# Performance work log

Measured on AMD Instinct MI355X. Metric: run time of the kernel, lower is better.

The kernel has to match this reference:

```python
import jax, jax.numpy as jnp
import numpy as np

DIM_MODEL = 1024
NUM_HEADS = 16
DIM_HEAD = 64
B, S = 2, 2048


def setup_inputs() -> dict:
    key = jax.random.key(0)
    ks = jax.random.split(key, 10)
    scale = 1.0 / np.sqrt(DIM_MODEL)
    inp = {
        "x": jax.random.normal(ks[0], (B, S, DIM_MODEL), dtype=jnp.float32),
        "padding_mask": jax.random.randint(ks[1], (B, S), 0, 2, dtype=jnp.int32),
        "Wq": jax.random.normal(ks[2], (DIM_MODEL, DIM_MODEL), dtype=jnp.float32) * scale,
        "bq": jnp.zeros((DIM_MODEL,), dtype=jnp.float32),
        "Wk": jax.random.normal(ks[3], (DIM_MODEL, DIM_MODEL), dtype=jnp.float32) * scale,
        "bk": jnp.zeros((DIM_MODEL,), dtype=jnp.float32),
        "Wv": jax.random.normal(ks[4], (DIM_MODEL, DIM_MODEL), dtype=jnp.float32) * scale,
        "bv": jnp.zeros((DIM_MODEL,), dtype=jnp.float32),
        "Wo": jax.random.normal(ks[5], (DIM_MODEL, DIM_MODEL), dtype=jnp.float32) * scale,
        "bo": jnp.zeros((DIM_MODEL,), dtype=jnp.float32),
    }
    return inp


def reference(x, padding_mask, Wq, bq, Wk, bk, Wv, bv, Wo, bo):
    b, s, _ = x.shape
    dot_scale = jnp.sqrt(jnp.asarray(DIM_HEAD, dtype=x.dtype))
    # projections -> (b, h, s, d)
    q = (x @ Wq + bq).reshape(b, s, NUM_HEADS, DIM_HEAD).transpose(0, 2, 1, 3)
    k = (x @ Wk + bk).reshape(b, s, NUM_HEADS, DIM_HEAD).transpose(0, 2, 1, 3)
    v = (x @ Wv + bv).reshape(b, s, NUM_HEADS, DIM_HEAD).transpose(0, 2, 1, 3)
    # scores (b, h, s, s)
    scores = jnp.einsum("bhqd,bhkd->bhqk", q, k) / dot_scale
    mask = (padding_mask == 1)[:, None, None, :]  # (b,1,1,s) over key positions
    scores = jnp.where(mask, -jnp.inf, scores)
    attn = jax.nn.softmax(scores, axis=-1)
    out = jnp.einsum("bhqk,bhkd->bhqd", attn, v)
    out = out.transpose(0, 2, 1, 3).reshape(b, s, NUM_HEADS * DIM_HEAD)
    return out @ Wo + bo
```

## Files before the change

kernel.cpp:

```cpp
#include <hip/hip_runtime.h>
#include <hip/hip_bf16.h>
#include <stdint.h>
#include <math.h>

#define D_MODEL 1024
#define NHEAD   16
#define DHEAD   64
#define BATCH   2
#define SEQ     2048
#define M_TOK   (BATCH * SEQ)

#define QSCALE 0.18033688011112042f

typedef __attribute__((ext_vector_type(8))) short   short8;
typedef __attribute__((ext_vector_type(8))) __bf16  bf16x8;
typedef __attribute__((ext_vector_type(4))) float   f32x4;

__device__ inline short f2bf(float f) {
  unsigned int u = __builtin_bit_cast(unsigned int, f);
  unsigned int r = (u + 0x7FFFu + ((u >> 16) & 1u)) >> 16;
  return (short)(unsigned short)r;
}
__device__ inline short f2bf_fast(float f) {
  unsigned int u = __builtin_bit_cast(unsigned int, f);
  return (short)(unsigned short)((u + 0x8000u) >> 16);
}

__device__ inline void gl_lds16(const void* g, void* l) {
  __builtin_amdgcn_global_load_lds((__attribute__((address_space(1))) void*)(g),
                                   (__attribute__((address_space(3))) void*)(l),
                                   16, 0, 0);
}

__device__ inline bf16x8 lds_frag(const short* p) {
  return *(const bf16x8*)(p);
}
__device__ inline bf16x8 lds_frag64(const short* p) {
  union { bf16x8 v; short4 h[2]; } u;
  u.h[0] = *(const short4*)(p);
  u.h[1] = *(const short4*)(p + 4);
  return u.v;
}

__global__ __launch_bounds__(256) void prep(const float* __restrict__ x,
                                            short* __restrict__ xb,
                                            const float* __restrict__ w0,
                                            const float* __restrict__ w1,
                                            const float* __restrict__ w2,
                                            const float* __restrict__ w3,
                                            short* __restrict__ out) {
  const int t = threadIdx.x;
  if (blockIdx.z == 4) {
    size_t base = ((size_t)blockIdx.y * 16 + blockIdx.x) * 16384;
    const float* in = x + base;
    short* o = xb + base;
#pragma unroll
    for (int i = 0; i < 16; ++i) {
      f32x4 v = *(const f32x4*)(in + (size_t)t * 4 + i * 1024);
      short4 s4;
      s4.x = f2bf(v[0]); s4.y = f2bf(v[1]); s4.z = f2bf(v[2]); s4.w = f2bf(v[3]);
      *(short4*)(o + (size_t)t * 4 + i * 1024) = s4;
    }
    return;
  }
  __shared__ short tile[64][72];
  const float* W = blockIdx.z == 0 ? w0 : blockIdx.z == 1 ? w1 : blockIdx.z == 2 ? w2 : w3;
  short* O = out + (size_t)blockIdx.z * (D_MODEL * (size_t)D_MODEL);
  int n0 = blockIdx.x * 64, k0 = blockIdx.y * 64;
#pragma unroll
  for (int i = 0; i < 16; ++i) {
    int idx = t + 256 * i;
    int r = idx >> 6, c = idx & 63;
    tile[r][c] = f2bf(W[(size_t)(k0 + r) * D_MODEL + n0 + c]);
  }
  __syncthreads();
#pragma unroll
  for (int i = 0; i < 16; ++i) {
    int idx = t + 256 * i;
    int r = idx >> 6, c = idx & 63;
    O[(size_t)(n0 + r) * D_MODEL + k0 + c] = tile[c][r];
  }
}

template <bool OUTF32, bool VT, int TN>
__global__ __launch_bounds__(256) void gemm128(const short* __restrict__ A,
                                               const short* __restrict__ Bt_base,
                                               const float* __restrict__ b0,
                                               const float* __restrict__ b1,
                                               const float* __restrict__ b2,
                                               void* __restrict__ out_base,
                                               short* __restrict__ vt,
                                               const int* __restrict__ pm) {
  constexpr int NI = TN / 32;
  const int z = blockIdx.z;
  const short* Bt   = Bt_base + (size_t)z * (D_MODEL * (size_t)D_MODEL);
  const float* bias = (z == 0) ? b0 : (z == 1) ? b1 : b2;

  __shared__ short As[128 * 64];
  __shared__ short Bs[TN * 64];

  const int t = threadIdx.x;
  const int lane = t & 63;
  const int wid = t >> 6;
  const int wm = (wid >> 1) * 64, wn = (wid & 1) * (TN / 2);
  const int m0 = blockIdx.x * 128, n0 = blockIdx.y * TN;
  const int cl = lane & 15, q = lane >> 4;
  const int sw = cl & 7;

  f32x4 acc[4][NI];
#pragma unroll
  for (int i = 0; i < 4; ++i)
#pragma unroll
    for (int j = 0; j < NI; ++j) acc[i][j] = 0.0f;

  for (int k0 = 0; k0 < D_MODEL; k0 += 64) {
    __syncthreads();
#pragma unroll
    for (int i = 0; i < 4; ++i) {
      int c = t + 256 * i;
      int row = c >> 3, cp = c & 7;
      int col = ((cp ^ (row & 7)) * 8);
      gl_lds16(A + (size_t)(m0 + row) * D_MODEL + k0 + col, (void*)(As + c * 8));
    }
#pragma unroll
    for (int i = 0; i < NI; ++i) {
      int c = t + 256 * i;
      int row = c >> 3, cp = c & 7;
      int col = ((cp ^ (row & 7)) * 8);
      gl_lds16(Bt + (size_t)(n0 + row) * D_MODEL + k0 + col, (void*)(Bs + c * 8));
    }
    __syncthreads();

    bf16x8 af[4][2], bfr[NI][2];
#pragma unroll
    for (int mi = 0; mi < 4; ++mi) {
      af[mi][0] = lds_frag(As + (wm + mi * 16 + cl) * 64 + (q ^ sw) * 8);
      af[mi][1] = lds_frag(As + (wm + mi * 16 + cl) * 64 + ((4 + q) ^ sw) * 8);
    }
#pragma unroll
    for (int ni = 0; ni < NI; ++ni) {
      bfr[ni][0] = lds_frag(Bs + (wn + ni * 16 + cl) * 64 + (q ^ sw) * 8);
      bfr[ni][1] = lds_frag(Bs + (wn + ni * 16 + cl) * 64 + ((4 + q) ^ sw) * 8);
    }
#pragma unroll
    for (int mi = 0; mi < 4; ++mi)
#pragma unroll
      for (int ni = 0; ni < NI; ++ni) {
        acc[mi][ni] = __builtin_amdgcn_mfma_f32_16x16x32_bf16(af[mi][0], bfr[ni][0], acc[mi][ni], 0, 0, 0);
        acc[mi][ni] = __builtin_amdgcn_mfma_f32_16x16x32_bf16(af[mi][1], bfr[ni][1], acc[mi][ni], 0, 0, 0);
      }
  }

  const float oscale = (VT && z == 0) ? QSCALE : 1.0f;
  int4 mm[4];
  if (VT && z == 2) {
#pragma unroll
    for (int mi = 0; mi < 4; ++mi) {
      int rbase = m0 + wm + mi * 16 + q * 4;
      mm[mi] = *(const int4*)(pm + (size_t)(rbase >> 11) * SEQ + (rbase & (SEQ - 1)));
    }
  }
#pragma unroll
  for (int ni = 0; ni < NI; ++ni) {
    int col = n0 + wn + ni * 16 + cl;
    float bv = bias[col];
#pragma unroll
    for (int mi = 0; mi < 4; ++mi) {
      int rbase = m0 + wm + mi * 16 + q * 4;
      if (VT && z == 2) {
        short4 o4;
        o4.x = (mm[mi].x == 1) ? (short)0 : f2bf_fast(acc[mi][ni][0] + bv);
        o4.y = (mm[mi].y == 1) ? (short)0 : f2bf_fast(acc[mi][ni][1] + bv);
        o4.z = (mm[mi].z == 1) ? (short)0 : f2bf_fast(acc[mi][ni][2] + bv);
        o4.w = (mm[mi].w == 1) ? (short)0 : f2bf_fast(acc[mi][ni][3] + bv);
        int btok = rbase >> 11;
        int s    = rbase & (SEQ - 1);
        *(short4*)(vt + (size_t)btok * ((size_t)D_MODEL * SEQ) + (size_t)col * SEQ + s) = o4;
      } else {
#pragma unroll
        for (int r = 0; r < 4; ++r) {
          float v = (acc[mi][ni][r] + bv) * oscale;
          size_t idx = (size_t)(rbase + r) * D_MODEL + col;
          if (OUTF32) {
            ((float*)out_base)[idx] = v;
          } else {
            short* out = (short*)out_base + (size_t)z * ((size_t)M_TOK * D_MODEL);
            out[idx] = f2bf_fast(v);
          }
        }
      }
    }
  }
}

__global__ __launch_bounds__(512) void attn_flash(const short* __restrict__ Q,
                                                  const short* __restrict__ K,
                                                  const short* __restrict__ Vt,
                                                  const int*   __restrict__ mask,
                                                  short* __restrict__ ctx) {
  const int qb = blockIdx.x;
  const int h  = blockIdx.y;
  const int b  = blockIdx.z;

  __shared__ __align__(16) short QPs[17408];
  __shared__ __align__(16) short Ks[2 * 64 * 64];
  __shared__ __align__(16) short Vts[2 * 64 * 64];
  __shared__ __align__(16) short Usall[SEQ];

  const int t = threadIdx.x;
  const int lane = t & 63;
  const int wid = t >> 6;
  const int wg  = wid >> 1;
  const int kvh = wid & 1;
  const int cl = lane & 15, q = lane >> 4;
  const int sw = cl & 7;

  const size_t rowQ0 = (size_t)b * SEQ + (size_t)qb * 128;
  const size_t rowK0 = (size_t)b * SEQ;
  const size_t vbase = ((size_t)b * D_MODEL + h * DHEAD) * SEQ;

  const int srow = t >> 3, scp = t & 7;
  const int scol = (scp ^ (srow & 7)) * 8;
  const short* Kg0 = K + (rowK0 + srow) * D_MODEL + h * DHEAD + scol;
  const short* Kg1 = K + (rowK0 + 1024 + srow) * D_MODEL + h * DHEAD + scol;
  const short* Vg0 = Vt + vbase + (size_t)srow * SEQ + scol;
  const short* Vg1 = Vt + vbase + (size_t)srow * SEQ + 1024 + scol;

  short8 gk0 = *(const short8*)(Kg0);
  short8 gk1 = *(const short8*)(Kg1);
  short8 gv0 = *(const short8*)(Vg0);
  short8 gv1 = *(const short8*)(Vg1);

#pragma unroll
  for (int i = 0; i < 4; ++i) {
    int idx = t + 512 * i;
    Usall[idx] = (mask[(size_t)b * SEQ + idx] == 1) ? (short)0 : (short)0x3F80;
  }

#pragma unroll
  for (int i = 0; i < 2; ++i) {
    int c = t + 512 * i;
    int row = c >> 3, cp = c & 7;
    gl_lds16(Q + (rowQ0 + row) * D_MODEL + h * DHEAD + ((cp ^ (row & 7)) * 8),
             (void*)(QPs + c * 8));
  }
  __syncthreads();

  bf16x8 qf[2][2];
#pragma unroll
  for (int rb = 0; rb < 2; ++rb) {
    int row = wg * 32 + rb * 16 + cl;
    qf[rb][0] = lds_frag(QPs + row * 64 + (q ^ sw) * 8);
    qf[rb][1] = lds_frag(QPs + row * 64 + ((4 + q) ^ sw) * 8);
  }
  short* Psw = QPs + wid * (32 * 68);
  const short* Kp = Ks  + kvh * 4096;
  const short* Vp = Vts + kvh * 4096;

  f32x4 lacc[2], oacc[2][4];
#pragma unroll
  for (int rb = 0; rb < 2; ++rb) {
    lacc[rb] = 0.0f;
#pragma unroll
    for (int dj = 0; dj < 4; ++dj) oacc[rb][dj] = 0.0f;
  }

  for (int s0 = 0; s0 < 1024; s0 += 64) {
    __syncthreads();

    *(short8*)(Ks  + t * 8)        = gk0;
    *(short8*)(Ks  + 4096 + t * 8) = gk1;
    *(short8*)(Vts + t * 8)        = gv0;
    *(short8*)(Vts + 4096 + t * 8) = gv1;
    __syncthreads();

    if (s0 + 64 < 1024) {
      int sn = s0 + 64;
      gk0 = *(const short8*)(Kg0 + (size_t)sn * D_MODEL);
      gk1 = *(const short8*)(Kg1 + (size_t)sn * D_MODEL);
      gv0 = *(const short8*)(Vg0 + sn);
      gv1 = *(const short8*)(Vg1 + sn);
    }

    const short* Up = Usall + kvh * 1024 + s0;

    f32x4 s[2][4];
#pragma unroll
    for (int j = 0; j < 4; ++j) {
      bf16x8 kf0 = lds_frag(Kp + (j * 16 + cl) * 64 + (q ^ sw) * 8);
      bf16x8 kf1 = lds_frag(Kp + (j * 16 + cl) * 64 + ((4 + q) ^ sw) * 8);
#pragma unroll
      for (int rb = 0; rb < 2; ++rb) {
        f32x4 sa = 0.0f;
        sa = __builtin_amdgcn_mfma_f32_16x16x32_bf16(qf[rb][0], kf0, sa, 0, 0, 0);
        sa = __builtin_amdgcn_mfma_f32_16x16x32_bf16(qf[rb][1], kf1, sa, 0, 0, 0);
        s[rb][j] = sa;
      }
    }

#pragma unroll
    for (int rb = 0; rb < 2; ++rb)
#pragma unroll
      for (int j = 0; j < 4; ++j)
#pragma unroll
        for (int r = 0; r < 4; ++r)
          Psw[(rb * 16 + q * 4 + r) * 68 + j * 16 + cl] =
              f2bf_fast(__builtin_amdgcn_exp2f(s[rb][j][r]));

    asm volatile("" ::: "memory");

    bf16x8 pf[2][2];
#pragma unroll
    for (int rb = 0; rb < 2; ++rb) {
      pf[rb][0] = lds_frag64(Psw + (rb * 16 + cl) * 68 + q * 8);
      pf[rb][1] = lds_frag64(Psw + (rb * 16 + cl) * 68 + 32 + q * 8);
    }
    bf16x8 uf0 = lds_frag(Up + q * 8);
    bf16x8 uf1 = lds_frag(Up + 32 + q * 8);
#pragma unroll
    for (int dj = 0; dj < 4; ++dj) {
      bf16x8 vf0 = lds_frag(Vp + (dj * 16 + cl) * 64 + (q ^ sw) * 8);
      bf16x8 vf1 = lds_frag(Vp + (dj * 16 + cl) * 64 + ((4 + q) ^ sw) * 8);
#pragma unroll
      for (int rb = 0; rb < 2; ++rb) {
        oacc[rb][dj] = __builtin_amdgcn_mfma_f32_16x16x32_bf16(pf[rb][0], vf0, oacc[rb][dj], 0, 0, 0);
        oacc[rb][dj] = __builtin_amdgcn_mfma_f32_16x16x32_bf16(pf[rb][1], vf1, oacc[rb][dj], 0, 0, 0);
      }
    }
#pragma unroll
    for (int rb = 0; rb < 2; ++rb) {
      lacc[rb] = __builtin_amdgcn_mfma_f32_16x16x32_bf16(pf[rb][0], uf0, lacc[rb], 0, 0, 0);
      lacc[rb] = __builtin_amdgcn_mfma_f32_16x16x32_bf16(pf[rb][1], uf1, lacc[rb], 0, 0, 0);
    }
  }

  __syncthreads();
  float* redO = (float*)QPs;
  float* redL = (float*)Ks;
  const int rbase = (wg * 64 + lane) * 32;
  const int lbase = (wg * 64 + lane) * 8;
  if (kvh) {
#pragma unroll
    for (int rb = 0; rb < 2; ++rb) {
#pragma unroll
      for (int dj = 0; dj < 4; ++dj) {
        int qi = (rb * 4 + dj) ^ (lane & 7);
        *(f32x4*)(redO + rbase + qi * 4) = oacc[rb][dj];
      }
      *(f32x4*)(redL + lbase + rb * 4) = lacc[rb];
    }
  }
  __syncthreads();
  if (kvh) return;
#pragma unroll
  for (int rb = 0; rb < 2; ++rb) {
    lacc[rb] += *(const f32x4*)(redL + lbase + rb * 4);
#pragma unroll
    for (int dj = 0; dj < 4; ++dj) {
      int qi = (rb * 4 + dj) ^ (lane & 7);
      oacc[rb][dj] += *(const f32x4*)(redO + rbase + qi * 4);
    }
  }

#pragma unroll
  for (int rb = 0; rb < 2; ++rb)
#pragma unroll
    for (int dj = 0; dj < 4; ++dj)
#pragma unroll
      for (int r = 0; r < 4; ++r) {
        float lv = lacc[rb][r];
        float o = (lv > 0.0f) ? oacc[rb][dj][r] / lv : 0.0f;
        size_t row = rowQ0 + wg * 32 + rb * 16 + q * 4 + r;
        ctx[row * D_MODEL + h * DHEAD + dj * 16 + cl] = f2bf(o);
      }
}

extern "C" void kernel_launch(void* const* d_in, const int* in_sizes, int n_in,
                              void* d_out, int out_size, void* d_ws, size_t ws_size,
                              hipStream_t stream) {
  (void)in_sizes; (void)n_in; (void)out_size; (void)ws_size;

  const float* x  = (const float*)d_in[0];
  const int*   pm = (const int*)  d_in[1];
  const float* Wq = (const float*)d_in[2];
  const float* bq = (const float*)d_in[3];
  const float* Wk = (const float*)d_in[4];
  const float* bk = (const float*)d_in[5];
  const float* Wv = (const float*)d_in[6];
  const float* bv = (const float*)d_in[7];
  const float* Wo = (const float*)d_in[8];
  const float* bo = (const float*)d_in[9];

  const size_t WMAT = (size_t)D_MODEL * D_MODEL;
  const size_t TOKD = (size_t)M_TOK * D_MODEL;

  short* base = (short*)d_ws;
  short* Wt = base;
  short* xb = base + 4 * WMAT;
  short* Qw = xb + TOKD;
  short* Kw = Qw + TOKD;
  short* Vtw = Kw + TOKD;
  short* Cw = Vtw + TOKD;

  prep<<<dim3(16, 16, 5), 256, 0, stream>>>(x, xb, Wq, Wk, Wv, Wo, Wt);
  gemm128<false, true, 128><<<dim3(M_TOK / 128, D_MODEL / 128, 3), 256, 0, stream>>>(
      xb, Wt, bq, bk, bv, Qw, Vtw, pm);
  attn_flash<<<dim3(SEQ / 128, NHEAD, BATCH), 512, 0, stream>>>(Qw, Kw, Vtw, pm, Cw);
  gemm128<true, false, 64><<<dim3(M_TOK / 128, D_MODEL / 64, 1), 256, 0, stream>>>(
      Cw, Wt + 3 * WMAT, bo, bo, bo, d_out, nullptr, nullptr);
}
```

Before: 209.5 us.

## Keep softmax probabilities in registers via transposed MFMA operand order

```diff
diff --git a/kernel.cpp b/kernel.cpp
--- a/kernel.cpp
+++ b/kernel.cpp
@@ -35,10 +35,10 @@
 __device__ inline bf16x8 lds_frag(const short* p) {
   return *(const bf16x8*)(p);
 }
-__device__ inline bf16x8 lds_frag64(const short* p) {
+__device__ inline bf16x8 lds_frag2x64(const short* p1, const short* p2) {
   union { bf16x8 v; short4 h[2]; } u;
-  u.h[0] = *(const short4*)(p);
-  u.h[1] = *(const short4*)(p + 4);
+  u.h[0] = *(const short4*)(p1);
+  u.h[1] = *(const short4*)(p2);
   return u.v;
 }
 
@@ -202,10 +202,11 @@
   const int h  = blockIdx.y;
   const int b  = blockIdx.z;
 
-  __shared__ __align__(16) short QPs[17408];
-  __shared__ __align__(16) short Ks[2 * 64 * 64];
-  __shared__ __align__(16) short Vts[2 * 64 * 64];
-  __shared__ __align__(16) short Usall[SEQ];
+  __shared__ __align__(16) short smem[28672];
+  short* Qs  = smem;
+  short* Ks  = smem + 8192;
+  short* Vts = smem + 16384;
+  float* Usf = (float*)(smem + 24576);
 
   const int t = threadIdx.x;
   const int lane = t & 63;
@@ -231,10 +232,14 @@
   short8 gv0 = *(const short8*)(Vg0);
   short8 gv1 = *(const short8*)(Vg1);
 
-#pragma unroll
-  for (int i = 0; i < 4; ++i) {
-    int idx = t + 512 * i;
-    Usall[idx] = (mask[(size_t)b * SEQ + idx] == 1) ? (short)0 : (short)0x3F80;
+  {
+    int4 mv = *(const int4*)(mask + (size_t)b * SEQ + t * 4);
+    f32x4 u4;
+    u4[0] = (mv.x == 1) ? 0.0f : 1.0f;
+    u4[1] = (mv.y == 1) ? 0.0f : 1.0f;
+    u4[2] = (mv.z == 1) ? 0.0f : 1.0f;
+    u4[3] = (mv.w == 1) ? 0.0f : 1.0f;
+    *(f32x4*)(Usf + t * 4) = u4;
   }
 
 #pragma unroll
@@ -242,7 +247,7 @@
     int c = t + 512 * i;
     int row = c >> 3, cp = c & 7;
     gl_lds16(Q + (rowQ0 + row) * D_MODEL + h * DHEAD + ((cp ^ (row & 7)) * 8),
-             (void*)(QPs + c * 8));
+             (void*)(Qs + c * 8));
   }
   __syncthreads();
 
@@ -250,12 +255,12 @@
 #pragma unroll
   for (int rb = 0; rb < 2; ++rb) {
     int row = wg * 32 + rb * 16 + cl;
-    qf[rb][0] = lds_frag(QPs + row * 64 + (q ^ sw) * 8);
-    qf[rb][1] = lds_frag(QPs + row * 64 + ((4 + q) ^ sw) * 8);
-  }
-  short* Psw = QPs + wid * (32 * 68);
+    qf[rb][0] = lds_frag(Qs + row * 64 + (q ^ sw) * 8);
+    qf[rb][1] = lds_frag(Qs + row * 64 + ((4 + q) ^ sw) * 8);
+  }
   const short* Kp = Ks  + kvh * 4096;
   const short* Vp = Vts + kvh * 4096;
+  const float* Up = Usf + kvh * 1024;
 
   f32x4 lacc[2], oacc[2][4];
 #pragma unroll
@@ -282,8 +287,6 @@
       gv1 = *(const short8*)(Vg1 + sn);
     }
 
-    const short* Up = Usall + kvh * 1024 + s0;
-
     f32x4 s[2][4];
 #pragma unroll
     for (int j = 0; j < 4; ++j) {
@@ -292,87 +295,111 @@
 #pragma unroll
       for (int rb = 0; rb < 2; ++rb) {
         f32x4 sa = 0.0f;
-        sa = __builtin_amdgcn_mfma_f32_16x16x32_bf16(qf[rb][0], kf0, sa, 0, 0, 0);
-        sa = __builtin_amdgcn_mfma_f32_16x16x32_bf16(qf[rb][1], kf1, sa, 0, 0, 0);
+        sa = __builtin_amdgcn_mfma_f32_16x16x32_bf16(kf0, qf[rb][0], sa, 0, 0, 0);
+        sa = __builtin_amdgcn_mfma_f32_16x16x32_bf16(kf1, qf[rb][1], sa, 0, 0, 0);
         s[rb][j] = sa;
       }
     }
 
+    f32x4 uv[4];
+#pragma unroll
+    for (int j = 0; j < 4; ++j)
+      uv[j] = *(const f32x4*)(Up + s0 + j * 16 + 4 * q);
 #pragma unroll
     for (int rb = 0; rb < 2; ++rb)
 #pragma unroll
-      for (int j = 0; j < 4; ++j)
+      for (int j = 0; j < 4; ++j) {
 #pragma unroll
         for (int r = 0; r < 4; ++r)
-          Psw[(rb * 16 + q * 4 + r) * 68 + j * 16 + cl] =
-              f2bf_fast(__builtin_amdgcn_exp2f(s[rb][j][r]));
-
-    asm volatile("" ::: "memory");
+          s[rb][j][r] = __builtin_amdgcn_exp2f(s[rb][j][r]) * uv[j][r];
+        lacc[rb] += s[rb][j];
+      }
 
     bf16x8 pf[2][2];
 #pragma unroll
-    for (int rb = 0; rb < 2; ++rb) {
-      pf[rb][0] = lds_frag64(Psw + (rb * 16 + cl) * 68 + q * 8);
-      pf[rb][1] = lds_frag64(Psw + (rb * 16 + cl) * 68 + 32 + q * 8);
-    }
-    bf16x8 uf0 = lds_frag(Up + q * 8);
-    bf16x8 uf1 = lds_frag(Up + 32 + q * 8);
+    for (int rb = 0; rb < 2; ++rb)
+#pragma unroll
+      for (int c = 0; c < 2; ++c) {
+        bf16x8 v;
+        v[0] = (__bf16)s[rb][2 * c][0];
+        v[1] = (__bf16)s[rb][2 * c][1];
+        v[2] = (__bf16)s[rb][2 * c][2];
+        v[3] = (__bf16)s[rb][2 * c][3];
+        v[4] = (__bf16)s[rb][2 * c + 1][0];
+        v[5] = (__bf16)s[rb][2 * c + 1][1];
+        v[6] = (__bf16)s[rb][2 * c + 1][2];
+        v[7] = (__bf16)s[rb][2 * c + 1][3];
+        pf[rb][c] = v;
+      }
+
+    const int vo = (q & 1) * 4;
 #pragma unroll
     for (int dj = 0; dj < 4; ++dj) {
-      bf16x8 vf0 = lds_frag(Vp + (dj * 16 + cl) * 64 + (q ^ sw) * 8);
-      bf16x8 vf1 = lds_frag(Vp + (dj * 16 + cl) * 64 + ((4 + q) ^ sw) * 8);
-#pragma unroll
-      for (int rb = 0; rb < 2; ++rb) {
-        oacc[rb][dj] = __builtin_amdgcn_mfma_f32_16x16x32_bf16(pf[rb][0], vf0, oacc[rb][dj], 0, 0, 0);
-        oacc[rb][dj] = __builtin_amdgcn_mfma_f32_16x16x32_bf16(pf[rb][1], vf1, oacc[rb][dj], 0, 0, 0);
-      }
-    }
-#pragma unroll
-    for (int rb = 0; rb < 2; ++rb) {
-      lacc[rb] = __builtin_amdgcn_mfma_f32_16x16x32_bf16(pf[rb][0], uf0, lacc[rb], 0, 0, 0);
-      lacc[rb] = __builtin_amdgcn_mfma_f32_16x16x32_bf16(pf[rb][1], uf1, lacc[rb], 0, 0, 0);
+      const short* vrow = Vp + (dj * 16 + cl) * 64;
+#pragma unroll
+      for (int c = 0; c < 2; ++c) {
+        int L1 = 4 * c + (q >> 1);
+        int L2 = L1 + 2;
+        bf16x8 vfc = lds_frag2x64(vrow + (L1 ^ sw) * 8 + vo,
+                                  vrow + (L2 ^ sw) * 8 + vo);
+#pragma unroll
+        for (int rb = 0; rb < 2; ++rb)
+          oacc[rb][dj] = __builtin_amdgcn_mfma_f32_16x16x32_bf16(vfc, pf[rb][c], oacc[rb][dj], 0, 0, 0);
+      }
     }
   }
 
   __syncthreads();
-  float* redO = (float*)QPs;
-  float* redL = (float*)Ks;
-  const int rbase = (wg * 64 + lane) * 32;
-  const int lbase = (wg * 64 + lane) * 8;
+  float hl[2];
+#pragma unroll
+  for (int rb = 0; rb < 2; ++rb)
+    hl[rb] = lacc[rb][0] + lacc[rb][1] + lacc[rb][2] + lacc[rb][3];
+
+  float* redO = (float*)smem;
+  float* redL = (float*)(smem + 16384);
+  const int slot = wg * 64 + lane;
   if (kvh) {
 #pragma unroll
     for (int rb = 0; rb < 2; ++rb) {
 #pragma unroll
       for (int dj = 0; dj < 4; ++dj) {
         int qi = (rb * 4 + dj) ^ (lane & 7);
-        *(f32x4*)(redO + rbase + qi * 4) = oacc[rb][dj];
-      }
-      *(f32x4*)(redL + lbase + rb * 4) = lacc[rb];
+        *(f32x4*)(redO + slot * 32 + qi * 4) = oacc[rb][dj];
+      }
+      redL[slot * 2 + rb] = hl[rb];
     }
   }
   __syncthreads();
   if (kvh) return;
 #pragma unroll
   for (int rb = 0; rb < 2; ++rb) {
-    lacc[rb] += *(const f32x4*)(redL + lbase + rb * 4);
+    hl[rb] += redL[slot * 2 + rb];
 #pragma unroll
     for (int dj = 0; dj < 4; ++dj) {
       int qi = (rb * 4 + dj) ^ (lane & 7);
-      oacc[rb][dj] += *(const f32x4*)(redO + rbase + qi * 4);
-    }
-  }
-
-#pragma unroll
-  for (int rb = 0; rb < 2; ++rb)
-#pragma unroll
-    for (int dj = 0; dj < 4; ++dj)
-#pragma unroll
-      for (int r = 0; r < 4; ++r) {
-        float lv = lacc[rb][r];
-        float o = (lv > 0.0f) ? oacc[rb][dj][r] / lv : 0.0f;
-        size_t row = rowQ0 + wg * 32 + rb * 16 + q * 4 + r;
-        ctx[row * D_MODEL + h * DHEAD + dj * 16 + cl] = f2bf(o);
-      }
+      oacc[rb][dj] += *(const f32x4*)(redO + slot * 32 + qi * 4);
+    }
+  }
+#pragma unroll
+  for (int rb = 0; rb < 2; ++rb) {
+    hl[rb] += __shfl_xor(hl[rb], 16);
+    hl[rb] += __shfl_xor(hl[rb], 32);
+  }
+
+#pragma unroll
+  for (int rb = 0; rb < 2; ++rb) {
+    float inv = (hl[rb] > 0.0f) ? 1.0f / hl[rb] : 0.0f;
+    size_t row = rowQ0 + wg * 32 + rb * 16 + cl;
+#pragma unroll
+    for (int dj = 0; dj < 4; ++dj) {
+      short4 o4;
+      o4.x = f2bf(oacc[rb][dj][0] * inv);
+      o4.y = f2bf(oacc[rb][dj][1] * inv);
+      o4.z = f2bf(oacc[rb][dj][2] * inv);
+      o4.w = f2bf(oacc[rb][dj][3] * inv);
+      *(short4*)(ctx + row * D_MODEL + h * DHEAD + dj * 16 + q * 4) = o4;
+    }
+  }
 }
 
 extern "C" void kernel_launch(void* const* d_in, const int* in_sizes, int n_in,
```

Result: no change. 207.9 us (-0.8%).
